# Kernel tuning notes

Hardware: AMD Instinct MI355X
Metric: run time of the kernel (lower is better)

## Reference

```python
import jax, jax.numpy as jnp
import numpy as np
import math

B, S, D, H = 2, 2048, 1024, 16
DK = D // H


def setup_inputs() -> dict:
    key = jax.random.key(0)
    ks = jax.random.split(key, 5)
    scale = 0.02
    x = jax.random.normal(ks[0], (B, S, D), dtype=jnp.float32)
    wq = jax.random.normal(ks[1], (D, D), dtype=jnp.float32) * scale
    wk = jax.random.normal(ks[2], (D, D), dtype=jnp.float32) * scale
    wv = jax.random.normal(ks[3], (D, D), dtype=jnp.float32) * scale
    wo = jax.random.normal(ks[4], (D, D), dtype=jnp.float32) * scale
    bq = jnp.zeros((D,), jnp.float32)
    bk = jnp.zeros((D,), jnp.float32)
    bv = jnp.zeros((D,), jnp.float32)
    bo = jnp.zeros((D,), jnp.float32)
    # causal mask: mask==0 positions are filled with -inf in the original
    mask = jnp.tril(jnp.ones((S, S), dtype=bool))[None, None]  # [1,1,S,S]
    return {"x": x, "mask": mask, "wq": wq, "bq": bq, "wk": wk, "bk": bk,
            "wv": wv, "bv": bv, "wo": wo, "bo": bo}


def reference(x, mask, wq, bq, wk, bk, wv, bv, wo, bo):
    b, sl, d = x.shape
    # torch Linear: y = x @ W^T + b
    def proj(w, bias):
        y = jnp.einsum('bsd,ed->bse', x, w) + bias
        return y.reshape(b, sl, H, DK).transpose(0, 2, 1, 3)  # [B,H,S,DK]
    q = proj(wq, bq)
    k = proj(wk, bk)
    v = proj(wv, bv)
    sc = jnp.einsum('bhqd,bhkd->bhqk', q, k) / math.sqrt(DK)  # [B,H,S,S]
    sc = jnp.where(mask, sc, -jnp.inf)
    aw = jax.nn.softmax(sc, axis=-1)
    # dropout is identity in eval mode (reference baseline)
    ao = jnp.einsum('bhqk,bhkd->bhqd', aw, v)
    ao = ao.transpose(0, 2, 1, 3).reshape(b, sl, d)
    out = jnp.einsum('bsd,ed->bse', ao, wo) + bo
    return out
```

## Files before the change

### kernel.cpp

```cpp
#include <hip/hip_runtime.h>
#include <cstdint>
#include <cstddef>

#define Bb 2
#define Ss 2048
#define Dd 1024
#define Hh 16
#define DKk 64

typedef unsigned short ushort_t;
typedef __bf16 bf16x8 __attribute__((ext_vector_type(8)));
typedef float f32x4 __attribute__((ext_vector_type(4)));
typedef unsigned short us8 __attribute__((ext_vector_type(8)));
typedef unsigned short us4 __attribute__((ext_vector_type(4)));

__device__ __forceinline__ ushort_t f2bf(float f) {
  __bf16 h = (__bf16)f;
  return __builtin_bit_cast(unsigned short, h);
}

__device__ __forceinline__ void gload_lds16(const void* g, void* l) {
  __builtin_amdgcn_global_load_lds(
      (__attribute__((address_space(1))) void*)(g),
      (__attribute__((address_space(3))) void*)(l),
      16, 0, 0);
}

__global__ __launch_bounds__(256) void cast_k(const float* __restrict__ s,
                                              ushort_t* __restrict__ d, int n8) {
  const int i = blockIdx.x * 256 + threadIdx.x;
  if (i >= n8) return;
  const float4* sp = (const float4*)s;
  float4 a = sp[2 * i], b = sp[2 * i + 1];
  us8 o;
  o[0] = f2bf(a.x); o[1] = f2bf(a.y); o[2] = f2bf(a.z); o[3] = f2bf(a.w);
  o[4] = f2bf(b.x); o[5] = f2bf(b.y); o[6] = f2bf(b.z); o[7] = f2bf(b.w);
  ((us8*)d)[i] = o;
}

template <int MODE>
__global__ __launch_bounds__(256) void gemm_k(
    const ushort_t* __restrict__ A, const ushort_t* __restrict__ W,
    const float* __restrict__ b0, const float* __restrict__ b1,
    const float* __restrict__ b2,
    ushort_t* __restrict__ oQ, ushort_t* __restrict__ oK,
    ushort_t* __restrict__ oVT, float* __restrict__ oF) {
  constexpr int Kd = 1024;
  __shared__ ushort_t As[128 * 32];
  __shared__ ushort_t Bs[128 * 32];
  const int tid = threadIdx.x;
  const int lane = tid & 63;
  const int wave = tid >> 6;
  const int m0 = blockIdx.y * 128;
  const int n0 = blockIdx.x * 128;
  const int lr = lane & 15;
  const int lg = lane >> 4;
  const int srow = lane >> 2;
  const int scol = (lane & 3) * 8;
  const int ar = (wave >> 1) * 64;
  const int bc = (wave & 1) * 64;

  f32x4 acc[4][4] = {};

  for (int kt = 0; kt < Kd / 32; ++kt) {
    const int k0 = kt * 32;
#pragma unroll
    for (int c = 0; c < 2; ++c) {
      const int seg = wave * 2 + c;
      const int row = seg * 16 + srow;
      gload_lds16(A + (size_t)(m0 + row) * Kd + k0 + scol, (char*)As + seg * 1024);
      gload_lds16(W + (size_t)(n0 + row) * Kd + k0 + scol, (char*)Bs + seg * 1024);
    }
    __syncthreads();
    bf16x8 af[4], bfr[4];
#pragma unroll
    for (int i = 0; i < 4; ++i)
      af[i] = *(const bf16x8*)&As[(ar + i * 16 + lr) * 32 + lg * 8];
#pragma unroll
    for (int j = 0; j < 4; ++j)
      bfr[j] = *(const bf16x8*)&Bs[(bc + j * 16 + lr) * 32 + lg * 8];
#pragma unroll
    for (int i = 0; i < 4; ++i)
#pragma unroll
      for (int j = 0; j < 4; ++j)
        acc[i][j] = __builtin_amdgcn_mfma_f32_16x16x32_bf16(af[i], bfr[j],
                                                            acc[i][j], 0, 0, 0);
    __syncthreads();
  }

#pragma unroll
  for (int i = 0; i < 4; ++i) {
    const int mrow = m0 + ar + i * 16 + lg * 4;
#pragma unroll
    for (int j = 0; j < 4; ++j) {
      const int n = n0 + bc + j * 16 + lr;
      if (MODE == 0) {
        const int sel = n >> 10;
        const int nn = n & 1023;
        const float bias = (sel == 0 ? b0 : sel == 1 ? b1 : b2)[nn];
        const int h = nn >> 6, dk = nn & 63;
        const int bidx = mrow >> 11;
        const int s = mrow & 2047;
        const int bh = bidx * Hh + h;
        if (sel == 2) {
          us4 pk;
#pragma unroll
          for (int r = 0; r < 4; ++r) pk[r] = f2bf(acc[i][j][r] + bias);
          *(us4*)&oVT[((size_t)bh * DKk + dk) * Ss + s] = pk;
        } else {
          ushort_t* dst = (sel == 0) ? oQ : oK;
          const float mul = (sel == 0) ? 0.1803368842f : 1.0f;
#pragma unroll
          for (int r = 0; r < 4; ++r)
            dst[((size_t)bh * Ss + (s + r)) * DKk + dk] =
                f2bf((acc[i][j][r] + bias) * mul);
        }
      } else {
        const float bias = b0[n];
#pragma unroll
        for (int r = 0; r < 4; ++r)
          oF[(size_t)(mrow + r) * Dd + n] = acc[i][j][r] + bias;
      }
    }
  }
}

__global__ __launch_bounds__(256, 4) void attn_k(const ushort_t* __restrict__ Qg,
                                                 const ushort_t* __restrict__ Kg,
                                                 const ushort_t* __restrict__ Vt,
                                                 ushort_t* __restrict__ AO) {
  __shared__ ushort_t Ks[2][64 * 64];
  __shared__ ushort_t Pl[4][16 * 72];
  const int tid = threadIdx.x, lane = tid & 63, wave = tid >> 6;
  const int bx = blockIdx.x;
  const int bh = bx & 31;
  const int r_ = bx >> 8;
  const int sub = (bx >> 5) & 7;
  const int g = (3 - r_) * 8 + ((r_ & 1) ? 7 - sub : sub);
  const int lr = lane & 15, lg = lane >> 4;
  const ushort_t* Qp = Qg + (size_t)bh * Ss * DKk;
  const ushort_t* Kp = Kg + (size_t)bh * Ss * DKk;
  const ushort_t* Vp = Vt + (size_t)bh * DKk * Ss;
  ushort_t* P = Pl[wave];
  const int s_row = lane >> 3;
  const int s_slot = (lane & 7) ^ s_row;
  const int sw = lr & 7;
  const int q0 = g * 64 + wave * 16;
  const int nt = g + 1;

  auto stageK = [&](int t, int buf) {
    const int rb = wave * 16;
#pragma unroll
    for (int c = 0; c < 2; ++c)
      gload_lds16(Kp + (size_t)(t * 64 + rb + c * 8 + s_row) * DKk + s_slot * 8,
                  &Ks[buf][(rb + c * 8) * 64]);
  };

  stageK(0, 0);

  bf16x8 qf[2];
#pragma unroll
  for (int ks = 0; ks < 2; ++ks)
    qf[ks] = *(const bf16x8*)&Qp[(size_t)(q0 + lr) * DKk + ks * 32 + lg * 8];

  bf16x8 onesv;
#pragma unroll
  for (int e = 0; e < 8; ++e) onesv[e] = (__bf16)1.0f;

  f32x4 o[4] = {};
  f32x4 l4 = {};
  float m_ = -3e38f;

  __syncthreads();

  for (int t = 0; t < nt; ++t) {
    const int cb = t & 1;
    if (t + 1 < nt) stageK(t + 1, cb ^ 1);
    const int j0 = t * 64;
    const bool diag = (t == nt - 1);
    const int nct = diag ? wave + 1 : 4;

    bf16x8 vt[4][2];
#pragma unroll
    for (int dj = 0; dj < 4; ++dj)
#pragma unroll
      for (int ksp = 0; ksp < 2; ++ksp)
        vt[dj][ksp] = *(const bf16x8*)&Vp[(size_t)(dj * 16 + lr) * Ss + j0 +
                                          ksp * 32 + lg * 8];

    f32x4 sc[4];
#pragma unroll
    for (int ct = 0; ct < 4; ++ct) {
      if (ct < nct) {
        const int krow = ct * 16 + lr;
        const bf16x8 k0v = *(const bf16x8*)&Ks[cb][krow * 64 + ((lg ^ sw) * 8)];
        const bf16x8 k1v =
            *(const bf16x8*)&Ks[cb][krow * 64 + (((4 | lg) ^ sw) * 8)];
        f32x4 z = {};
        z = __builtin_amdgcn_mfma_f32_16x16x32_bf16(k0v, qf[0], z, 0, 0, 0);
        z = __builtin_amdgcn_mfma_f32_16x16x32_bf16(k1v, qf[1], z, 0, 0, 0);
        sc[ct] = z;
      }
    }
    if (diag) {
#pragma unroll
      for (int ct = 0; ct < 4; ++ct)
        if (ct == nct - 1)
#pragma unroll
          for (int r = 0; r < 4; ++r)
            if (lg * 4 + r > lr) sc[ct][r] = -1e30f;
    }

    float mx = -3e38f;
#pragma unroll
    for (int ct = 0; ct < 4; ++ct)
      if (ct < nct)
#pragma unroll
        for (int r = 0; r < 4; ++r) mx = fmaxf(mx, sc[ct][r]);
    mx = fmaxf(mx, __shfl_xor(mx, 16, 64));
    mx = fmaxf(mx, __shfl_xor(mx, 32, 64));
    const float mnew = fmaxf(m_, mx);
    const float fs = __builtin_exp2f(m_ - mnew);
    m_ = mnew;
#pragma unroll
    for (int ct = 0; ct < 4; ++ct) {
      if (ct < nct) {
        float p0 = __builtin_exp2f(sc[ct][0] - m_);
        float p1 = __builtin_exp2f(sc[ct][1] - m_);
        float p2 = __builtin_exp2f(sc[ct][2] - m_);
        float p3 = __builtin_exp2f(sc[ct][3] - m_);
        us4 pk;
        pk[0] = f2bf(p0); pk[1] = f2bf(p1); pk[2] = f2bf(p2); pk[3] = f2bf(p3);
        *(us4*)&P[lr * 72 + ct * 16 + lg * 4] = pk;
      } else {
        us4 zz = {};
        *(us4*)&P[lr * 72 + ct * 16 + lg * 4] = zz;
      }
    }

#pragma unroll
    for (int dj = 0; dj < 4; ++dj)
#pragma unroll
      for (int r = 0; r < 4; ++r) o[dj][r] *= fs;
    l4[0] *= fs;

    asm volatile("s_waitcnt lgkmcnt(0)" ::: "memory");
    bf16x8 pa[2];
#pragma unroll
    for (int ksp = 0; ksp < 2; ++ksp)
      pa[ksp] = *(const bf16x8*)&P[lr * 72 + ksp * 32 + lg * 8];

#pragma unroll
    for (int ksp = 0; ksp < 2; ++ksp)
      l4 = __builtin_amdgcn_mfma_f32_16x16x32_bf16(onesv, pa[ksp], l4, 0, 0, 0);
#pragma unroll
    for (int dj = 0; dj < 4; ++dj)
#pragma unroll
      for (int ksp = 0; ksp < 2; ++ksp)
        o[dj] = __builtin_amdgcn_mfma_f32_16x16x32_bf16(vt[dj][ksp], pa[ksp],
                                                        o[dj], 0, 0, 0);

    __syncthreads();
  }

  const int bb = bh >> 4, hh = bh & 15;
  const float inv = 1.0f / l4[0];
#pragma unroll
  for (int dj = 0; dj < 4; ++dj) {
    us4 pk;
#pragma unroll
    for (int r = 0; r < 4; ++r) pk[r] = f2bf(o[dj][r] * inv);
    *(us4*)&AO[((size_t)bb * Ss + q0 + lr) * Dd + hh * 64 + dj * 16 + lg * 4] =
        pk;
  }
}

extern "C" void kernel_launch(void* const* d_in, const int* in_sizes, int n_in,
                              void* d_out, int out_size, void* d_ws, size_t ws_size,
                              hipStream_t stream) {
  const float* x  = (const float*)d_in[0];
  const float* wq = (const float*)d_in[2];
  const float* bq = (const float*)d_in[3];
  const float* wk = (const float*)d_in[4];
  const float* bk = (const float*)d_in[5];
  const float* wv = (const float*)d_in[6];
  const float* bv = (const float*)d_in[7];
  const float* wo = (const float*)d_in[8];
  const float* bo = (const float*)d_in[9];

  ushort_t* ws   = (ushort_t*)d_ws;
  ushort_t* xb   = ws;
  ushort_t* wqkv = xb + 4096 * 1024;
  ushort_t* wob  = wqkv + 3072 * 1024;
  ushort_t* Qb   = wob + 1024 * 1024;
  ushort_t* Kb   = Qb + 4194304;
  ushort_t* VTb  = Kb + 4194304;
  ushort_t* AOb  = xb;

  cast_k<<<2048, 256, 0, stream>>>(x, xb, 524288);
  cast_k<<<512, 256, 0, stream>>>(wq, wqkv, 131072);
  cast_k<<<512, 256, 0, stream>>>(wk, wqkv + 1048576, 131072);
  cast_k<<<512, 256, 0, stream>>>(wv, wqkv + 2097152, 131072);
  cast_k<<<512, 256, 0, stream>>>(wo, wob, 131072);

  gemm_k<0><<<dim3(24, 32), 256, 0, stream>>>(xb, wqkv, bq, bk, bv, Qb, Kb, VTb,
                                              nullptr);
  attn_k<<<1024, 256, 0, stream>>>(Qb, Kb, VTb, AOb);
  gemm_k<1><<<dim3(8, 32), 256, 0, stream>>>(AOb, wob, bo, nullptr, nullptr,
                                             nullptr, nullptr, nullptr,
                                             (float*)d_out);
}
```

Measured before the change: 151.7 us.

## Split attention into 32-row query blocks and merge weight cast kernels

```diff
diff --git a/kernel.cpp b/kernel.cpp
--- a/kernel.cpp
+++ b/kernel.cpp
@@ -36,6 +36,22 @@
   o[0] = f2bf(a.x); o[1] = f2bf(a.y); o[2] = f2bf(a.z); o[3] = f2bf(a.w);
   o[4] = f2bf(b.x); o[5] = f2bf(b.y); o[6] = f2bf(b.z); o[7] = f2bf(b.w);
   ((us8*)d)[i] = o;
+}
+
+__global__ __launch_bounds__(256) void castw_k(const float* __restrict__ s0,
+                                               const float* __restrict__ s1,
+                                               const float* __restrict__ s2,
+                                               const float* __restrict__ s3,
+                                               ushort_t* __restrict__ d) {
+  const int w = blockIdx.x >> 9;
+  const int i = (blockIdx.x & 511) * 256 + threadIdx.x;
+  const float* s = (w == 0) ? s0 : (w == 1) ? s1 : (w == 2) ? s2 : s3;
+  const float4* sp = (const float4*)s;
+  float4 a = sp[2 * i], b = sp[2 * i + 1];
+  us8 o;
+  o[0] = f2bf(a.x); o[1] = f2bf(a.y); o[2] = f2bf(a.z); o[3] = f2bf(a.w);
+  o[4] = f2bf(b.x); o[5] = f2bf(b.y); o[6] = f2bf(b.z); o[7] = f2bf(b.w);
+  ((us8*)(d + (size_t)w * 1048576))[i] = o;
 }
 
 template <int MODE>
@@ -125,18 +141,16 @@
   }
 }
 
-__global__ __launch_bounds__(256, 4) void attn_k(const ushort_t* __restrict__ Qg,
+__global__ __launch_bounds__(128, 4) void attn_k(const ushort_t* __restrict__ Qg,
                                                  const ushort_t* __restrict__ Kg,
                                                  const ushort_t* __restrict__ Vt,
                                                  ushort_t* __restrict__ AO) {
   __shared__ ushort_t Ks[2][64 * 64];
-  __shared__ ushort_t Pl[4][16 * 72];
+  __shared__ ushort_t Pl[2][16 * 72];
   const int tid = threadIdx.x, lane = tid & 63, wave = tid >> 6;
   const int bx = blockIdx.x;
   const int bh = bx & 31;
-  const int r_ = bx >> 8;
-  const int sub = (bx >> 5) & 7;
-  const int g = (3 - r_) * 8 + ((r_ & 1) ? 7 - sub : sub);
+  const int g32 = 63 - (bx >> 5);
   const int lr = lane & 15, lg = lane >> 4;
   const ushort_t* Qp = Qg + (size_t)bh * Ss * DKk;
   const ushort_t* Kp = Kg + (size_t)bh * Ss * DKk;
@@ -145,13 +159,14 @@
   const int s_row = lane >> 3;
   const int s_slot = (lane & 7) ^ s_row;
   const int sw = lr & 7;
-  const int q0 = g * 64 + wave * 16;
-  const int nt = g + 1;
+  const int q0 = g32 * 32 + wave * 16;
+  const int nt = (g32 >> 1) + 1;
+  const int nctd = wave + ((g32 & 1) << 1) + 1;
 
   auto stageK = [&](int t, int buf) {
-    const int rb = wave * 16;
-#pragma unroll
-    for (int c = 0; c < 2; ++c)
+    const int rb = wave * 32;
+#pragma unroll
+    for (int c = 0; c < 4; ++c)
       gload_lds16(Kp + (size_t)(t * 64 + rb + c * 8 + s_row) * DKk + s_slot * 8,
                   &Ks[buf][(rb + c * 8) * 64]);
   };
@@ -178,7 +193,7 @@
     if (t + 1 < nt) stageK(t + 1, cb ^ 1);
     const int j0 = t * 64;
     const bool diag = (t == nt - 1);
-    const int nct = diag ? wave + 1 : 4;
+    const int nct = diag ? nctd : 4;
 
     bf16x8 vt[4][2];
 #pragma unroll
@@ -298,14 +313,11 @@
   ushort_t* AOb  = xb;
 
   cast_k<<<2048, 256, 0, stream>>>(x, xb, 524288);
-  cast_k<<<512, 256, 0, stream>>>(wq, wqkv, 131072);
-  cast_k<<<512, 256, 0, stream>>>(wk, wqkv + 1048576, 131072);
-  cast_k<<<512, 256, 0, stream>>>(wv, wqkv + 2097152, 131072);
-  cast_k<<<512, 256, 0, stream>>>(wo, wob, 131072);
+  castw_k<<<2048, 256, 0, stream>>>(wq, wk, wv, wo, wqkv);
 
   gemm_k<0><<<dim3(24, 32), 256, 0, stream>>>(xb, wqkv, bq, bk, bv, Qb, Kb, VTb,
                                               nullptr);
-  attn_k<<<1024, 256, 0, stream>>>(Qb, Kb, VTb, AOb);
+  attn_k<<<2048, 128, 0, stream>>>(Qb, Kb, VTb, AOb);
   gemm_k<1><<<dim3(8, 32), 256, 0, stream>>>(AOb, wob, bo, nullptr, nullptr,
                                              nullptr, nullptr, nullptr,
                                              (float*)d_out);
```

Result: no change. 149.7 us (-1.4%).
